# Kernel tuning notes

Measured on AMD Instinct MI355X. Metric: run time of the kernel, lower is better.

Reference implementation:

```python
import jax, jax.numpy as jnp
import numpy as np

EMB = 512
N_LAYERS = 8
N_HEADS = 16
FF_MULT = 4
NUM_PATCHES = 196
B = 32
N_VIS = 49
LN_EPS = 1e-5


def _sincos_1d(embed_dim, pos):
    omega = np.arange(embed_dim // 2, dtype=np.float64)
    omega /= embed_dim / 2.0
    omega = 1.0 / 10000 ** omega
    pos = pos.reshape(-1)
    out = np.einsum('m,d->md', pos, omega)
    return np.concatenate([np.sin(out), np.cos(out)], axis=1)


def _sincos_2d(embed_dim, grid_size):
    grid_h = np.arange(grid_size, dtype=np.float32)
    grid_w = np.arange(grid_size, dtype=np.float32)
    grid = np.stack(np.meshgrid(grid_w, grid_h), axis=0).reshape([2, 1, grid_size, grid_size])
    emb_h = _sincos_1d(embed_dim // 2, grid[0])
    emb_w = _sincos_1d(embed_dim // 2, grid[1])
    return np.concatenate([emb_h, emb_w], axis=1)


def setup_inputs() -> dict:
    key = jax.random.key(0)
    ks = jax.random.split(key, 20)
    D, H, FF, L = EMB, N_HEADS, FF_MULT * EMB, N_LAYERS
    s = 0.02
    inp = {}
    inp['x_enc_out_vis'] = jax.random.normal(ks[0], (B, N_VIS + 1, D), dtype=jnp.float32)
    # per-batch permutation of [0, NUM_PATCHES)
    u = jax.random.uniform(ks[1], (B, NUM_PATCHES))
    inp['idx_restore_patches'] = jnp.argsort(u, axis=1).astype(jnp.int32)
    inp['mask_token'] = jax.random.normal(ks[2], (1, 1, D), dtype=jnp.float32) * s
    inp['pos_emb'] = jnp.asarray(_sincos_2d(D, int(NUM_PATCHES ** 0.5))[None], dtype=jnp.float32)
    # stacked per-layer params, layout [in, out] (equivalent to torch Linear math)
    inp['Wq'] = jax.random.normal(ks[3], (L, D, D), dtype=jnp.float32) * s
    inp['bq'] = jnp.zeros((L, D), jnp.float32)
    inp['Wk'] = jax.random.normal(ks[4], (L, D, D), dtype=jnp.float32) * s
    inp['bk'] = jnp.zeros((L, D), jnp.float32)
    inp['Wv'] = jax.random.normal(ks[5], (L, D, D), dtype=jnp.float32) * s
    inp['bv'] = jnp.zeros((L, D), jnp.float32)
    inp['Wo'] = jax.random.normal(ks[6], (L, D, D), dtype=jnp.float32) * s
    inp['bo'] = jnp.zeros((L, D), jnp.float32)
    inp['ln1_g'] = jnp.ones((L, D), jnp.float32)
    inp['ln1_b'] = jnp.zeros((L, D), jnp.float32)
    inp['W1'] = jax.random.normal(ks[7], (L, D, FF), dtype=jnp.float32) * s
    inp['b1'] = jnp.zeros((L, FF), jnp.float32)
    inp['W2'] = jax.random.normal(ks[8], (L, FF, D), dtype=jnp.float32) * s
    inp['b2'] = jnp.zeros((L, D), jnp.float32)
    inp['ln2_g'] = jnp.ones((L, D), jnp.float32)
    inp['ln2_b'] = jnp.zeros((L, D), jnp.float32)
    inp['lnf_g'] = jnp.ones((D,), jnp.float32)
    inp['lnf_b'] = jnp.zeros((D,), jnp.float32)
    return inp


def _layernorm(x, g, b):
    m = jnp.mean(x, axis=-1, keepdims=True)
    v = jnp.mean((x - m) ** 2, axis=-1, keepdims=True)
    return (x - m) * jax.lax.rsqrt(v + LN_EPS) * g + b


def _decoder_forward(x_enc_out_vis, idx_restore, mask_token, pos_emb,
                     Wq, bq, Wk, bk, Wv, bv, Wo, bo, ln1_g, ln1_b,
                     W1, b1, W2, b2, ln2_g, ln2_b, lnf_g, lnf_b):
    Bsz, Nvis1, D = x_enc_out_vis.shape
    N = pos_emb.shape[1]
    H = N_HEADS
    hd = D // H
    # reassemble: visible patches (drop CLS) followed by mask tokens, then unshuffle
    vis = x_enc_out_vis[:, 1:]                                   # [B, Nvis, D]
    mtok = jnp.broadcast_to(mask_token, (Bsz, N - (Nvis1 - 1), D))
    shuffled = jnp.concatenate([vis, mtok], axis=1)              # [B, N, D]
    x = jnp.take_along_axis(shuffled, idx_restore[:, :, None], axis=1) + pos_emb

    def block(x, p):
        wq, bq_, wk, bk_, wv, bv_, wo, bo_, g1, be1, w1, bf1, w2, bf2, g2, be2 = p
        q = (x @ wq + bq_).reshape(Bsz, N, H, hd).transpose(0, 2, 1, 3)
        k = (x @ wk + bk_).reshape(Bsz, N, H, hd).transpose(0, 2, 1, 3)
        v = (x @ wv + bv_).reshape(Bsz, N, H, hd).transpose(0, 2, 1, 3)
        scores = jnp.einsum('bhqd,bhkd->bhqk', q, k) / jnp.sqrt(jnp.float32(hd))
        attn = jax.nn.softmax(scores, axis=-1)
        o = jnp.einsum('bhqk,bhkd->bhqd', attn, v)
        o = o.transpose(0, 2, 1, 3).reshape(Bsz, N, D)
        attended = o @ wo + bo_
        x = _layernorm(attended + x, g1, be1)
        ff = jax.nn.relu(x @ w1 + bf1) @ w2 + bf2
        x = _layernorm(ff + x, g2, be2)
        return x, None

    params = (Wq, bq, Wk, bk, Wv, bv, Wo, bo, ln1_g, ln1_b, W1, b1, W2, b2, ln2_g, ln2_b)
    x, _ = jax.lax.scan(block, x, params)
    return _layernorm(x, lnf_g, lnf_b)


def reference(x_enc_out_vis, idx_restore_patches, mask_token, pos_emb,
              Wq, bq, Wk, bk, Wv, bv, Wo, bo, ln1_g, ln1_b,
              W1, b1, W2, b2, ln2_g, ln2_b, lnf_g, lnf_b):
    return _decoder_forward(x_enc_out_vis, idx_restore_patches, mask_token, pos_emb,
                            Wq, bq, Wk, bk, Wv, bv, Wo, bo, ln1_g, ln1_b,
                            W1, b1, W2, b2, ln2_g, ln2_b, lnf_g, lnf_b)
```

## Files before the change

### kernel.cpp

```cpp
#include <hip/hip_runtime.h>

#define LAYERS 8
#define DIM 512
#define FFD 2048
#define NTOK 6272
#define NSEQ 196
#define BATCH 32
#define NHEAD 16
#define HD 32
#define NP 224
#define PSTRIDE 512

typedef unsigned short u16;
typedef __bf16 bf16x8 __attribute__((ext_vector_type(8)));
typedef float f32x4 __attribute__((ext_vector_type(4)));
typedef unsigned short u16x8 __attribute__((ext_vector_type(8)));

__device__ __forceinline__ u16 f2bf(float f) {
    unsigned u = __float_as_uint(f);
    u += 0x7FFF + ((u >> 16) & 1);
    return (u16)(u >> 16);
}
__device__ __forceinline__ float bf2f(u16 u) {
    return __uint_as_float((unsigned)u << 16);
}

typedef __attribute__((address_space(1))) void gvoid_t;
typedef __attribute__((address_space(3))) void lvoid_t;
__device__ __forceinline__ void gload_lds16(const void* g, void* l) {
    __builtin_amdgcn_global_load_lds((gvoid_t*)g, (lvoid_t*)l, 16, 0, 0);
}

__global__ __launch_bounds__(256) void transpose_w(const float* __restrict__ in,
                                                   u16* __restrict__ out, int K, int N) {
    __shared__ float t[32][33];
    size_t base = (size_t)blockIdx.z * K * N;
    int n0 = blockIdx.x * 32, k0 = blockIdx.y * 32;
    int tx = threadIdx.x, ty = threadIdx.y;
#pragma unroll
    for (int i = 0; i < 4; ++i)
        t[ty + i * 8][tx] = in[base + (size_t)(k0 + ty + i * 8) * N + n0 + tx];
    __syncthreads();
#pragma unroll
    for (int i = 0; i < 4; ++i)
        out[base + (size_t)(n0 + ty + i * 8) * K + k0 + tx] = f2bf(t[tx][ty + i * 8]);
}

__global__ void pack3_bias(const float* __restrict__ a, const float* __restrict__ b,
                           const float* __restrict__ c, float* __restrict__ o, int n) {
    int i = blockIdx.x * 256 + threadIdx.x;
    if (i < n) { o[i] = a[i]; o[n + i] = b[i]; o[2 * n + i] = c[i]; }
}

__global__ __launch_bounds__(128) void gather_pos(const float* __restrict__ xenc,
                                                  const int* __restrict__ idx,
                                                  const float* __restrict__ mtok,
                                                  const float* __restrict__ pos,
                                                  float* __restrict__ x, u16* __restrict__ xb) {
    int token = blockIdx.x;
    int b = token / NSEQ, t = token - b * NSEQ;
    int id = idx[token];
    const float* src = (id < 49) ? (xenc + ((size_t)b * 50 + id + 1) * DIM) : mtok;
    int d = threadIdx.x * 4;
    float4 s = *(const float4*)(src + d);
    float4 p = *(const float4*)(pos + (size_t)t * DIM + d);
    float4 r;
    r.x = s.x + p.x; r.y = s.y + p.y; r.z = s.z + p.z; r.w = s.w + p.w;
    *(float4*)(x + (size_t)token * DIM + d) = r;
    ushort4 rb;
    rb.x = f2bf(r.x); rb.y = f2bf(r.y); rb.z = f2bf(r.z); rb.w = f2bf(r.w);
    *(ushort4*)(xb + (size_t)token * DIM + d) = rb;
}

template<int EPI>
__global__ __launch_bounds__(256) void gemm4(
    const u16* __restrict__ A, int lda, long long zsA,
    const u16* __restrict__ Bt, int ldb, long long zsB,
    const float* __restrict__ bias, long long zsBias,
    u16* __restrict__ outB, long long zsOut,
    int N, int K) {
    __shared__ u16 As[128 * 64];
    __shared__ u16 Bs[128 * 64];
    int tid = threadIdx.x;
    int lane = tid & 63, wid = tid >> 6;
    int z = blockIdx.z;
    const u16* Az = A + (size_t)z * zsA;
    const u16* Bz = Bt + (size_t)z * zsB;
    int m0 = blockIdx.y * 128, n0 = blockIdx.x * 128;
    int l16 = lane & 15, kq = lane >> 4;
    int wm = (wid >> 1) * 64, wn = (wid & 1) * 64;

    f32x4 acc[4][4];
    f32x4 zero = {0.f, 0.f, 0.f, 0.f};
#pragma unroll
    for (int a = 0; a < 4; ++a)
#pragma unroll
        for (int b = 0; b < 4; ++b) acc[a][b] = zero;

    for (int k0 = 0; k0 < K; k0 += 64) {
        __syncthreads();
#pragma unroll
        for (int i = 0; i < 4; ++i) {
            int c = i * 256 + tid;
            int row = c >> 3;
            int kof = ((c & 7) * 16) ^ ((row & 7) << 4);
            gload_lds16((const char*)Az + ((size_t)(m0 + row) * lda + k0) * 2 + kof,
                        (char*)As + (size_t)c * 16);
            gload_lds16((const char*)Bz + ((size_t)(n0 + row) * ldb + k0) * 2 + kof,
                        (char*)Bs + (size_t)c * 16);
        }
        __syncthreads();

#pragma unroll
        for (int kh = 0; kh < 2; ++kh) {
            bf16x8 af[4], bfr[4];
#pragma unroll
            for (int mr = 0; mr < 4; ++mr) {
                int row = wm + mr * 16 + l16;
                int cb = (kh * 64 + kq * 16) ^ ((row & 7) << 4);
                af[mr] = *(const bf16x8*)((const char*)As + row * 128 + cb);
            }
#pragma unroll
            for (int nc = 0; nc < 4; ++nc) {
                int row = wn + nc * 16 + l16;
                int cb = (kh * 64 + kq * 16) ^ ((row & 7) << 4);
                bfr[nc] = *(const bf16x8*)((const char*)Bs + row * 128 + cb);
            }
#pragma unroll
            for (int mr = 0; mr < 4; ++mr)
#pragma unroll
                for (int nc = 0; nc < 4; ++nc)
                    acc[mr][nc] = __builtin_amdgcn_mfma_f32_16x16x32_bf16(af[mr], bfr[nc],
                                                                          acc[mr][nc], 0, 0, 0);
        }
    }

    const float* biasz = (EPI != 4) ? bias + (size_t)z * zsBias : nullptr;
#pragma unroll
    for (int mr = 0; mr < 4; ++mr)
#pragma unroll
        for (int nc = 0; nc < 4; ++nc)
#pragma unroll
            for (int i = 0; i < 4; ++i) {
                int rg = m0 + wm + mr * 16 + kq * 4 + i;
                int cg = n0 + wn + nc * 16 + l16;
                float v = acc[mr][nc][i];
                size_t off = (size_t)z * zsOut + (size_t)rg * N + cg;
                if (EPI == 1) { v += biasz[cg]; outB[off] = f2bf(v > 0.f ? v : 0.f); }
                else if (EPI == 3) { v += biasz[cg]; outB[off] = f2bf(v); }
                else outB[off] = f2bf(v);
            }
}

__global__ __launch_bounds__(256) void red_ln(const u16* __restrict__ p0, long long ps,
                                              const float* __restrict__ bias,
                                              const float* __restrict__ gg,
                                              const float* __restrict__ bb,
                                              float* __restrict__ x, u16* __restrict__ xb) {
    int t = blockIdx.x * 4 + (threadIdx.x >> 6);
    int lane = threadIdx.x & 63;
    size_t base = (size_t)t * DIM;
    int c0 = lane * 8;
    u16x8 pa = *(const u16x8*)(p0 + base + c0);
    u16x8 pb = *(const u16x8*)(p0 + ps + base + c0);
    float4 xa = *(const float4*)(x + base + c0);
    float4 xc = *(const float4*)(x + base + c0 + 4);
    float4 ba = *(const float4*)(bias + c0);
    float4 bc = *(const float4*)(bias + c0 + 4);
    float xs[8] = {xa.x, xa.y, xa.z, xa.w, xc.x, xc.y, xc.z, xc.w};
    float bs[8] = {ba.x, ba.y, ba.z, ba.w, bc.x, bc.y, bc.z, bc.w};
    float v[8];
    float s = 0.f, s2 = 0.f;
#pragma unroll
    for (int i = 0; i < 8; ++i) {
        v[i] = bf2f(pa[i]) + bf2f(pb[i]) + bs[i] + xs[i];
        s += v[i]; s2 += v[i] * v[i];
    }
#pragma unroll
    for (int off = 32; off; off >>= 1) { s += __shfl_xor(s, off); s2 += __shfl_xor(s2, off); }
    float m = s * (1.f / 512.f);
    float var = s2 * (1.f / 512.f) - m * m;
    float rs = rsqrtf(var + 1e-5f);
    float4 ga = *(const float4*)(gg + c0);
    float4 gc = *(const float4*)(gg + c0 + 4);
    float4 b0 = *(const float4*)(bb + c0);
    float4 b1 = *(const float4*)(bb + c0 + 4);
    float gs[8] = {ga.x, ga.y, ga.z, ga.w, gc.x, gc.y, gc.z, gc.w};
    float os[8] = {b0.x, b0.y, b0.z, b0.w, b1.x, b1.y, b1.z, b1.w};
    float o[8];
    u16x8 ob16;
#pragma unroll
    for (int i = 0; i < 8; ++i) {
        o[i] = (v[i] - m) * rs * gs[i] + os[i];
        ob16[i] = f2bf(o[i]);
    }
    float4 o0 = {o[0], o[1], o[2], o[3]};
    float4 o1 = {o[4], o[5], o[6], o[7]};
    *(float4*)(x + base + c0) = o0;
    *(float4*)(x + base + c0 + 4) = o1;
    *(u16x8*)(xb + base + c0) = ob16;
}

__global__ __launch_bounds__(256) void attn_mfma(const u16* __restrict__ qkvb,
                                                 u16* __restrict__ ob) {
    __shared__ u16 Ks[NP * 32];
    __shared__ u16 VTs[32 * 232];
    __shared__ u16 Ps[4][16 * (PSTRIDE / 2)];
    int bh = blockIdx.x;
    int b = bh >> 4, h = bh & 15;
    int tid = threadIdx.x, lane = tid & 63, wid = tid >> 6;
    int l16 = lane & 15, kq = lane >> 4;
    const size_t MS = (size_t)NTOK * DIM;
    const u16* qg = qkvb + ((size_t)b * NSEQ) * DIM + h * HD;
    const u16* kg = qg + MS;
    const u16* vg = qg + 2 * MS;

    for (int c = tid; c < 784; c += 256) {
        int row = c >> 2, ch = c & 3;
        gload_lds16(kg + (size_t)row * DIM + ch * 8, (char*)Ks + c * 16);
    }
    for (int i = tid; i < 448; i += 256) ((unsigned*)(Ks + 196 * 32))[i] = 0;
    for (int i = tid; i < 1568; i += 256) {
        int j = i >> 3, d0 = (i & 7) * 4;
        ushort4 vv = *(const ushort4*)(vg + (size_t)j * DIM + d0);
        VTs[(d0 + 0) * 232 + j] = vv.x;
        VTs[(d0 + 1) * 232 + j] = vv.y;
        VTs[(d0 + 2) * 232 + j] = vv.z;
        VTs[(d0 + 3) * 232 + j] = vv.w;
    }
    for (int i = tid; i < 1024; i += 256) {
        int d = i >> 5, j = 196 + (i & 31);
        VTs[d * 232 + j] = 0;
    }
    __syncthreads();

    const float scale = 0.17677669529663687f;
    char* psb = (char*)&Ps[wid][0];

    for (int p = wid; p < 13; p += 4) {
        int r0 = p * 16;
        int qrow = r0 + l16; if (qrow > 195) qrow = 195;
        bf16x8 qf = *(const bf16x8*)(qg + (size_t)qrow * DIM + kq * 8);

        f32x4 z4 = {0.f, 0.f, 0.f, 0.f};
        f32x4 s[14];
#pragma unroll
        for (int ct = 0; ct < 14; ++ct) {
            bf16x8 kf = *(const bf16x8*)&Ks[(ct * 16 + l16) * 32 + kq * 8];
            s[ct] = __builtin_amdgcn_mfma_f32_16x16x32_bf16(qf, kf, z4, 0, 0, 0);
        }
        bool v12 = (l16 < 4);
        float mx[4], sum[4], inv[4];
#pragma unroll
        for (int i = 0; i < 4; ++i) {
            float m = -1e30f;
#pragma unroll
            for (int ct = 0; ct < 12; ++ct) m = fmaxf(m, s[ct][i]);
            if (v12) m = fmaxf(m, s[12][i]);
            mx[i] = m * scale;
        }
#pragma unroll
        for (int off = 8; off; off >>= 1)
#pragma unroll
            for (int i = 0; i < 4; ++i) mx[i] = fmaxf(mx[i], __shfl_xor(mx[i], off));
#pragma unroll
        for (int i = 0; i < 4; ++i) sum[i] = 0.f;
#pragma unroll
        for (int ct = 0; ct < 14; ++ct)
#pragma unroll
            for (int i = 0; i < 4; ++i) {
                bool valid = (ct < 12) || (ct == 12 && v12);
                float e = valid ? __expf(s[ct][i] * scale - mx[i]) : 0.f;
                s[ct][i] = e;
                sum[i] += e;
            }
#pragma unroll
        for (int off = 8; off; off >>= 1)
#pragma unroll
            for (int i = 0; i < 4; ++i) sum[i] += __shfl_xor(sum[i], off);
#pragma unroll
        for (int i = 0; i < 4; ++i) inv[i] = 1.f / sum[i];

#pragma unroll
        for (int ct = 0; ct < 14; ++ct)
#pragma unroll
            for (int i = 0; i < 4; ++i) {
                int rl = kq * 4 + i;
                int byte = rl * PSTRIDE + (((ct * 16 + l16) * 2) ^ ((rl & 7) << 4));
                *(u16*)(psb + byte) = f2bf(s[ct][i]);
            }

        f32x4 o0 = {0.f, 0.f, 0.f, 0.f}, o1 = {0.f, 0.f, 0.f, 0.f};
#pragma unroll
        for (int kt = 0; kt < 7; ++kt) {
            int K2 = kt * 64 + kq * 16;
            bf16x8 pa = *(const bf16x8*)(psb + l16 * PSTRIDE + (K2 ^ ((l16 & 7) << 4)));
            bf16x8 va = *(const bf16x8*)&VTs[l16 * 232 + kt * 32 + kq * 8];
            bf16x8 vb = *(const bf16x8*)&VTs[(16 + l16) * 232 + kt * 32 + kq * 8];
            o0 = __builtin_amdgcn_mfma_f32_16x16x32_bf16(pa, va, o0, 0, 0, 0);
            o1 = __builtin_amdgcn_mfma_f32_16x16x32_bf16(pa, vb, o1, 0, 0, 0);
        }
#pragma unroll
        for (int i = 0; i < 4; ++i) {
            int row = r0 + kq * 4 + i;
            if (row < NSEQ) {
                size_t rb = ((size_t)b * NSEQ + row) * DIM + h * HD;
                ob[rb + l16] = f2bf(o0[i] * inv[i]);
                ob[rb + 16 + l16] = f2bf(o1[i] * inv[i]);
            }
        }
    }
}

__global__ __launch_bounds__(256) void ln_final(const float* __restrict__ y,
                                                const float* __restrict__ gg,
                                                const float* __restrict__ bb,
                                                float* __restrict__ xout) {
    int t = blockIdx.x * 4 + (threadIdx.x >> 6);
    int lane = threadIdx.x & 63;
    const float* row = y + (size_t)t * DIM;
    float4 a = *(const float4*)(row + lane * 4);
    float4 c = *(const float4*)(row + 256 + lane * 4);
    float s = a.x + a.y + a.z + a.w + c.x + c.y + c.z + c.w;
    float s2 = a.x * a.x + a.y * a.y + a.z * a.z + a.w * a.w
             + c.x * c.x + c.y * c.y + c.z * c.z + c.w * c.w;
#pragma unroll
    for (int off = 32; off; off >>= 1) { s += __shfl_xor(s, off); s2 += __shfl_xor(s2, off); }
    float m = s * (1.f / 512.f);
    float var = s2 * (1.f / 512.f) - m * m;
    float rs = rsqrtf(var + 1e-5f);
    float4 g0 = *(const float4*)(gg + lane * 4);
    float4 g1 = *(const float4*)(gg + 256 + lane * 4);
    float4 b0 = *(const float4*)(bb + lane * 4);
    float4 b1 = *(const float4*)(bb + 256 + lane * 4);
    float4 o0, o1;
    o0.x = (a.x - m) * rs * g0.x + b0.x;
    o0.y = (a.y - m) * rs * g0.y + b0.y;
    o0.z = (a.z - m) * rs * g0.z + b0.z;
    o0.w = (a.w - m) * rs * g0.w + b0.w;
    o1.x = (c.x - m) * rs * g1.x + b1.x;
    o1.y = (c.y - m) * rs * g1.y + b1.y;
    o1.z = (c.z - m) * rs * g1.z + b1.z;
    o1.w = (c.w - m) * rs * g1.w + b1.w;
    *(float4*)(xout + (size_t)t * DIM + lane * 4) = o0;
    *(float4*)(xout + (size_t)t * DIM + 256 + lane * 4) = o1;
}

extern "C" void kernel_launch(void* const* d_in, const int* in_sizes, int n_in,
                              void* d_out, int out_size, void* d_ws, size_t ws_size,
                              hipStream_t stream) {
    const float* xenc = (const float*)d_in[0];
    const int*   idxr = (const int*)d_in[1];
    const float* mtok = (const float*)d_in[2];
    const float* pos  = (const float*)d_in[3];
    const float* Wq = (const float*)d_in[4];  const float* bq = (const float*)d_in[5];
    const float* Wk = (const float*)d_in[6];  const float* bk = (const float*)d_in[7];
    const float* Wv = (const float*)d_in[8];  const float* bv = (const float*)d_in[9];
    const float* Wo = (const float*)d_in[10]; const float* bo = (const float*)d_in[11];
    const float* ln1g = (const float*)d_in[12]; const float* ln1b = (const float*)d_in[13];
    const float* W1 = (const float*)d_in[14]; const float* b1 = (const float*)d_in[15];
    const float* W2 = (const float*)d_in[16]; const float* b2 = (const float*)d_in[17];
    const float* ln2g = (const float*)d_in[18]; const float* ln2b = (const float*)d_in[19];
    const float* lnfg = (const float*)d_in[20]; const float* lnfb = (const float*)d_in[21];

    char* w = (char*)d_ws;
    u16* WTqkvo = (u16*)w; w += (size_t)4 * LAYERS * DIM * DIM * 2;
    u16* WT1    = (u16*)w; w += (size_t)LAYERS * DIM * FFD * 2;
    u16* WT2    = (u16*)w; w += (size_t)LAYERS * FFD * DIM * 2;
    float* bqkv = (float*)w; w += (size_t)3 * LAYERS * DIM * 4;
    float* x    = (float*)w; w += (size_t)NTOK * DIM * 4;
    u16*   xb   = (u16*)w;  w += (size_t)NTOK * DIM * 2;
    u16*   qkvb = (u16*)w;  w += (size_t)3 * NTOK * DIM * 2;
    u16*   ob   = (u16*)w;  w += (size_t)NTOK * DIM * 2;
    u16*   hb   = (u16*)w;  w += (size_t)NTOK * FFD * 2;
    size_t need = (size_t)(w - (char*)d_ws);
    if (ws_size < need) return;

    u16* pp = qkvb;
    const long long ND = (long long)NTOK * DIM;

    const size_t WL = (size_t)DIM * DIM;

    transpose_w<<<dim3(DIM / 32, DIM / 32, LAYERS), dim3(32, 8), 0, stream>>>(Wq, WTqkvo + 0 * (size_t)LAYERS * WL, DIM, DIM);
    transpose_w<<<dim3(DIM / 32, DIM / 32, LAYERS), dim3(32, 8), 0, stream>>>(Wk, WTqkvo + 1 * (size_t)LAYERS * WL, DIM, DIM);
    transpose_w<<<dim3(DIM / 32, DIM / 32, LAYERS), dim3(32, 8), 0, stream>>>(Wv, WTqkvo + 2 * (size_t)LAYERS * WL, DIM, DIM);
    transpose_w<<<dim3(DIM / 32, DIM / 32, LAYERS), dim3(32, 8), 0, stream>>>(Wo, WTqkvo + 3 * (size_t)LAYERS * WL, DIM, DIM);
    transpose_w<<<dim3(FFD / 32, DIM / 32, LAYERS), dim3(32, 8), 0, stream>>>(W1, WT1, DIM, FFD);
    transpose_w<<<dim3(DIM / 32, FFD / 32, LAYERS), dim3(32, 8), 0, stream>>>(W2, WT2, FFD, DIM);
    pack3_bias<<<(LAYERS * DIM + 255) / 256, 256, 0, stream>>>(bq, bk, bv, bqkv, LAYERS * DIM);

    gather_pos<<<NTOK, 128, 0, stream>>>(xenc, idxr, mtok, pos, x, xb);

    for (int l = 0; l < LAYERS; ++l) {
        gemm4<3><<<dim3(4, 49, 3), 256, 0, stream>>>(
            xb, DIM, 0, WTqkvo + l * WL, DIM, (long long)LAYERS * WL,
            bqkv + l * DIM, (long long)LAYERS * DIM,
            qkvb, ND, DIM, DIM);
        attn_mfma<<<BATCH * NHEAD, 256, 0, stream>>>(qkvb, ob);
        gemm4<4><<<dim3(4, 49, 2), 256, 0, stream>>>(
            ob, DIM, 256, WTqkvo + 3 * (size_t)LAYERS * WL + l * WL, DIM, 256,
            nullptr, 0, pp, ND, DIM, 256);
        red_ln<<<NTOK / 4, 256, 0, stream>>>(pp, ND, bo + l * DIM,
                                             ln1g + l * DIM, ln1b + l * DIM, x, xb);
        gemm4<1><<<dim3(16, 49, 1), 256, 0, stream>>>(
            xb, DIM, 0, WT1 + (size_t)l * DIM * FFD, DIM, 0,
            b1 + l * FFD, 0, hb, 0, FFD, DIM);
        gemm4<4><<<dim3(4, 49, 2), 256, 0, stream>>>(
            hb, FFD, 1024, WT2 + (size_t)l * FFD * DIM, FFD, 1024,
            nullptr, 0, pp, ND, DIM, 1024);
        red_ln<<<NTOK / 4, 256, 0, stream>>>(pp, ND, b2 + l * DIM,
                                             ln2g + l * DIM, ln2b + l * DIM, x, xb);
    }
    ln_final<<<NTOK / 4, 256, 0, stream>>>(x, lnfg, lnfb, (float*)d_out);
}
```

Measured before the change: 1.011 ms.

## Double-buffer GEMM LDS tiles and split attention query tiles across two blocks

```diff
diff --git a/kernel.cpp b/kernel.cpp
--- a/kernel.cpp
+++ b/kernel.cpp
@@ -9,7 +9,6 @@
 #define NHEAD 16
 #define HD 32
 #define NP 224
-#define PSTRIDE 512
 
 typedef unsigned short u16;
 typedef __bf16 bf16x8 __attribute__((ext_vector_type(8)));
@@ -79,8 +78,8 @@
     const float* __restrict__ bias, long long zsBias,
     u16* __restrict__ outB, long long zsOut,
     int N, int K) {
-    __shared__ u16 As[128 * 64];
-    __shared__ u16 Bs[128 * 64];
+    __shared__ u16 As[2][128 * 64];
+    __shared__ u16 Bs[2][128 * 64];
     int tid = threadIdx.x;
     int lane = tid & 63, wid = tid >> 6;
     int z = blockIdx.z;
@@ -97,20 +96,28 @@
 #pragma unroll
         for (int b = 0; b < 4; ++b) acc[a][b] = zero;
 
-    for (int k0 = 0; k0 < K; k0 += 64) {
-        __syncthreads();
-#pragma unroll
-        for (int i = 0; i < 4; ++i) {
-            int c = i * 256 + tid;
-            int row = c >> 3;
-            int kof = ((c & 7) * 16) ^ ((row & 7) << 4);
-            gload_lds16((const char*)Az + ((size_t)(m0 + row) * lda + k0) * 2 + kof,
-                        (char*)As + (size_t)c * 16);
-            gload_lds16((const char*)Bz + ((size_t)(n0 + row) * ldb + k0) * 2 + kof,
-                        (char*)Bs + (size_t)c * 16);
-        }
-        __syncthreads();
-
+#define STAGE(buf, kk)                                                             \
+    {                                                                              \
+        _Pragma("unroll")                                                          \
+        for (int i_ = 0; i_ < 4; ++i_) {                                           \
+            int c_ = i_ * 256 + tid;                                               \
+            int row_ = c_ >> 3;                                                    \
+            int kof_ = ((c_ & 7) * 16) ^ ((row_ & 7) << 4);                        \
+            gload_lds16((const char*)Az + ((size_t)(m0 + row_) * lda + (kk)) * 2 + kof_, \
+                        (char*)As[buf] + (size_t)c_ * 16);                         \
+            gload_lds16((const char*)Bz + ((size_t)(n0 + row_) * ldb + (kk)) * 2 + kof_, \
+                        (char*)Bs[buf] + (size_t)c_ * 16);                         \
+        }                                                                          \
+    }
+
+    int nk = K >> 6;
+    STAGE(0, 0);
+    __syncthreads();
+    for (int kt = 0; kt < nk; ++kt) {
+        int cur = kt & 1;
+        if (kt + 1 < nk) STAGE(cur ^ 1, (kt + 1) << 6);
+        const char* Ac = (const char*)As[cur];
+        const char* Bc = (const char*)Bs[cur];
 #pragma unroll
         for (int kh = 0; kh < 2; ++kh) {
             bf16x8 af[4], bfr[4];
@@ -118,13 +125,13 @@
             for (int mr = 0; mr < 4; ++mr) {
                 int row = wm + mr * 16 + l16;
                 int cb = (kh * 64 + kq * 16) ^ ((row & 7) << 4);
-                af[mr] = *(const bf16x8*)((const char*)As + row * 128 + cb);
+                af[mr] = *(const bf16x8*)(Ac + row * 128 + cb);
             }
 #pragma unroll
             for (int nc = 0; nc < 4; ++nc) {
                 int row = wn + nc * 16 + l16;
                 int cb = (kh * 64 + kq * 16) ^ ((row & 7) << 4);
-                bfr[nc] = *(const bf16x8*)((const char*)Bs + row * 128 + cb);
+                bfr[nc] = *(const bf16x8*)(Bc + row * 128 + cb);
             }
 #pragma unroll
             for (int mr = 0; mr < 4; ++mr)
@@ -133,7 +140,9 @@
                     acc[mr][nc] = __builtin_amdgcn_mfma_f32_16x16x32_bf16(af[mr], bfr[nc],
                                                                           acc[mr][nc], 0, 0, 0);
         }
-    }
+        __syncthreads();
+    }
+#undef STAGE
 
     const float* biasz = (EPI != 4) ? bias + (size_t)z * zsBias : nullptr;
 #pragma unroll
@@ -205,8 +214,8 @@
                                                  u16* __restrict__ ob) {
     __shared__ u16 Ks[NP * 32];
     __shared__ u16 VTs[32 * 232];
-    __shared__ u16 Ps[4][16 * (PSTRIDE / 2)];
-    int bh = blockIdx.x;
+    __shared__ u16 Ps[4][16 * 128];
+    int bh = blockIdx.x >> 1, half = blockIdx.x & 1;
     int b = bh >> 4, h = bh & 15;
     int tid = threadIdx.x, lane = tid & 63, wid = tid >> 6;
     int l16 = lane & 15, kq = lane >> 4;
@@ -236,8 +245,9 @@
 
     const float scale = 0.17677669529663687f;
     char* psb = (char*)&Ps[wid][0];
-
-    for (int p = wid; p < 13; p += 4) {
+    int pend = half ? 13 : 7;
+
+    for (int p = half * 7 + wid; p < pend; p += 4) {
         int r0 = p * 16;
         int qrow = r0 + l16; if (qrow > 195) qrow = 195;
         bf16x8 qf = *(const bf16x8*)(qg + (size_t)qrow * DIM + kq * 8);
@@ -281,20 +291,36 @@
 #pragma unroll
         for (int i = 0; i < 4; ++i) inv[i] = 1.f / sum[i];
 
-#pragma unroll
-        for (int ct = 0; ct < 14; ++ct)
+        f32x4 o0 = {0.f, 0.f, 0.f, 0.f}, o1 = {0.f, 0.f, 0.f, 0.f};
+#pragma unroll
+        for (int ct = 0; ct < 8; ++ct)
 #pragma unroll
             for (int i = 0; i < 4; ++i) {
                 int rl = kq * 4 + i;
-                int byte = rl * PSTRIDE + (((ct * 16 + l16) * 2) ^ ((rl & 7) << 4));
+                int byte = rl * 256 + (((ct * 16 + l16) * 2) ^ ((rl & 7) << 4));
                 *(u16*)(psb + byte) = f2bf(s[ct][i]);
             }
-
-        f32x4 o0 = {0.f, 0.f, 0.f, 0.f}, o1 = {0.f, 0.f, 0.f, 0.f};
-#pragma unroll
-        for (int kt = 0; kt < 7; ++kt) {
-            int K2 = kt * 64 + kq * 16;
-            bf16x8 pa = *(const bf16x8*)(psb + l16 * PSTRIDE + (K2 ^ ((l16 & 7) << 4)));
+#pragma unroll
+        for (int kt = 0; kt < 4; ++kt) {
+            int K2 = (kt * 64 + kq * 16) ^ ((l16 & 7) << 4);
+            bf16x8 pa = *(const bf16x8*)(psb + l16 * 256 + K2);
+            bf16x8 va = *(const bf16x8*)&VTs[l16 * 232 + kt * 32 + kq * 8];
+            bf16x8 vb = *(const bf16x8*)&VTs[(16 + l16) * 232 + kt * 32 + kq * 8];
+            o0 = __builtin_amdgcn_mfma_f32_16x16x32_bf16(pa, va, o0, 0, 0, 0);
+            o1 = __builtin_amdgcn_mfma_f32_16x16x32_bf16(pa, vb, o1, 0, 0, 0);
+        }
+#pragma unroll
+        for (int ct = 8; ct < 14; ++ct)
+#pragma unroll
+            for (int i = 0; i < 4; ++i) {
+                int rl = kq * 4 + i;
+                int byte = rl * 256 + ((((ct - 8) * 16 + l16) * 2) ^ ((rl & 7) << 4));
+                *(u16*)(psb + byte) = f2bf(s[ct][i]);
+            }
+#pragma unroll
+        for (int kt = 4; kt < 7; ++kt) {
+            int K2 = ((kt - 4) * 64 + kq * 16) ^ ((l16 & 7) << 4);
+            bf16x8 pa = *(const bf16x8*)(psb + l16 * 256 + K2);
             bf16x8 va = *(const bf16x8*)&VTs[l16 * 232 + kt * 32 + kq * 8];
             bf16x8 vb = *(const bf16x8*)&VTs[(16 + l16) * 232 + kt * 32 + kq * 8];
             o0 = __builtin_amdgcn_mfma_f32_16x16x32_bf16(pa, va, o0, 0, 0, 0);
@@ -396,7 +422,7 @@
             xb, DIM, 0, WTqkvo + l * WL, DIM, (long long)LAYERS * WL,
             bqkv + l * DIM, (long long)LAYERS * DIM,
             qkvb, ND, DIM, DIM);
-        attn_mfma<<<BATCH * NHEAD, 256, 0, stream>>>(qkvb, ob);
+        attn_mfma<<<BATCH * NHEAD * 2, 256, 0, stream>>>(qkvb, ob);
         gemm4<4><<<dim3(4, 49, 2), 256, 0, stream>>>(
             ob, DIM, 256, WTqkvo + 3 * (size_t)LAYERS * WL + l * WL, DIM, 256,
             nullptr, 0, pp, ND, DIM, 256);
```

Result: no change. 998.7 us (-1.2%).
